# Performance work log

Measured on AMD Instinct MI355X. Metric: run time of the kernel, lower is better.

The kernel has to match this reference:

```python
import jax, jax.numpy as jnp
import numpy as np

N_NODES = 50000
N_EDGES = 1_600_000
N_HEADS = 8
IN_DIM = 512
OUT_DIM = 64
LRELU_ALPHA = 0.2


def setup_inputs() -> dict:
    key = jax.random.key(0)
    k1, k2, k3, k4, k5 = jax.random.split(key, 5)
    x = jax.random.normal(k1, (N_NODES, IN_DIM), dtype=jnp.float32)
    # glorot-ish scale for weights
    W = jax.random.normal(k2, (N_HEADS, IN_DIM, OUT_DIM), dtype=jnp.float32) * (1.0 / np.sqrt(IN_DIM))
    att_w = jax.random.normal(k3, (N_HEADS, 2 * OUT_DIM), dtype=jnp.float32) * (1.0 / np.sqrt(2 * OUT_DIM))
    src = jax.random.randint(k4, (N_EDGES,), 0, N_NODES, dtype=jnp.int64 if jax.config.read('jax_enable_x64') else jnp.int32).astype(jnp.int32)
    dst = jax.random.randint(k5, (N_EDGES,), 0, N_NODES, dtype=jnp.int32)
    return {"x": x, "W": W, "att_w": att_w, "src": src, "dst": dst}


def reference(x, W, att_w, src, dst):
    # GAT forward (eval mode: dropout=0, bias off, heads concatenated).
    # attention score: leaky_relu([f_src || f_dst] @ a) == leaky_relu(a1.f_src + a2.f_dst)
    outs = []
    for h in range(N_HEADS):
        feat = x @ W[h]                               # [N, F]
        a1 = att_w[h, :OUT_DIM]                       # [F]
        a2 = att_w[h, OUT_DIM:]                       # [F]
        alpha_s = feat @ a1                           # [N]
        alpha_d = feat @ a2                           # [N]
        logit = jax.nn.leaky_relu(alpha_s[src] + alpha_d[dst], LRELU_ALPHA)  # [E]
        # sparse row-wise softmax over segments keyed by src (row index)
        m = jax.ops.segment_max(logit, src, num_segments=N_NODES)
        e = jnp.exp(logit - m[src])
        denom = jax.ops.segment_sum(e, src, num_segments=N_NODES)
        att = e / denom[src]                          # [E]
        # sparse-dense aggregation: out[row] = sum_edges att * feat[col]
        agg = jax.ops.segment_sum(att[:, None] * feat[dst], src, num_segments=N_NODES)  # [N, F]
        outs.append(jax.nn.relu(agg))                 # act per head (average_heads=False)
    return jnp.concatenate(outs, axis=1)              # [N, H*F]
```

## Files before the change

kernel.cpp:

```cpp
#include <hip/hip_runtime.h>
#include <math.h>

#define N_NODES   50000
#define N_EDGES   1600000
#define N_HEADS   8
#define IN_DIM    512
#define OUT_DIM   64
#define FEAT_DIM  512
#define LRELU_A   0.2f
#define M_TILES   391
#define M_PAD     (M_TILES*128)

typedef __attribute__((ext_vector_type(8))) short bf16x8;
typedef __attribute__((ext_vector_type(4))) float f32x4;

__device__ inline unsigned short f2bf(float f) {
    unsigned int u = __float_as_uint(f);
    u = (u + 0x7FFFu + ((u >> 16) & 1u)) >> 16;
    return (unsigned short)u;
}
__device__ inline float bf2f(short s) {
    return __uint_as_float(((unsigned int)(unsigned short)s) << 16);
}

__global__ __launch_bounds__(256) void convert_x(const float* __restrict__ x,
                                                 unsigned short* __restrict__ xh) {
    int i = blockIdx.x * blockDim.x + threadIdx.x;
    if (i >= N_NODES * IN_DIM / 4) return;
    float4 v = ((const float4*)x)[i];
    ushort4 o;
    o.x = f2bf(v.x); o.y = f2bf(v.y); o.z = f2bf(v.z); o.w = f2bf(v.w);
    ((ushort4*)xh)[i] = o;
}

__global__ __launch_bounds__(256) void prep_b(const float* __restrict__ W,
                                              unsigned short* __restrict__ Bt) {
    int t = blockIdx.x * blockDim.x + threadIdx.x;
    if (t >= FEAT_DIM * IN_DIM) return;
    int n = t >> 9, k = t & 511;
    int h = n >> 6, o = n & 63;
    Bt[t] = f2bf(W[(size_t)h * IN_DIM * OUT_DIM + (size_t)k * OUT_DIM + o]);
}

__global__ __launch_bounds__(256) void gemm_mfma(const unsigned short* __restrict__ xh,
                                                 const unsigned short* __restrict__ Bt,
                                                 unsigned short* __restrict__ feat_h) {
    __shared__ __align__(16) unsigned short As[128 * 32];
    __shared__ __align__(16) unsigned short Bs[128 * 32];
    const int t    = threadIdx.x;
    const int wid  = t >> 6;
    const int lane = t & 63;
    const int m0   = blockIdx.x * 128;
    const int n0   = blockIdx.y * 128;
    const int wm   = (wid >> 1) * 64;
    const int wn   = (wid & 1) * 64;
    const int mr   = lane & 15;
    const int q    = lane >> 4;

    f32x4 acc[4][4];
    #pragma unroll
    for (int i = 0; i < 4; ++i)
        #pragma unroll
        for (int j = 0; j < 4; ++j) acc[i][j] = 0.0f;

    const char* xb = (const char*)xh;
    const char* bb = (const char*)Bt;
    const int o1 = t * 16;         const int row1 = o1 >> 6, kb1 = o1 & 63;
    const int o2 = t * 16 + 4096;  const int row2 = o2 >> 6, kb2 = o2 & 63;
    char* lA1 = ((char*)As) + wid * 1024;
    char* lA2 = ((char*)As) + 4096 + wid * 1024;
    char* lB1 = ((char*)Bs) + wid * 1024;
    char* lB2 = ((char*)Bs) + 4096 + wid * 1024;

    for (int k0 = 0; k0 < IN_DIM; k0 += 32) {
        const int kbyte = k0 * 2;
        __builtin_amdgcn_global_load_lds(
            (const __attribute__((address_space(1))) unsigned int*)(xb + (size_t)(m0 + row1) * (IN_DIM * 2) + kbyte + kb1),
            (__attribute__((address_space(3))) unsigned int*)lA1, 16, 0, 0);
        __builtin_amdgcn_global_load_lds(
            (const __attribute__((address_space(1))) unsigned int*)(xb + (size_t)(m0 + row2) * (IN_DIM * 2) + kbyte + kb2),
            (__attribute__((address_space(3))) unsigned int*)lA2, 16, 0, 0);
        __builtin_amdgcn_global_load_lds(
            (const __attribute__((address_space(1))) unsigned int*)(bb + (size_t)(n0 + row1) * (IN_DIM * 2) + kbyte + kb1),
            (__attribute__((address_space(3))) unsigned int*)lB1, 16, 0, 0);
        __builtin_amdgcn_global_load_lds(
            (const __attribute__((address_space(1))) unsigned int*)(bb + (size_t)(n0 + row2) * (IN_DIM * 2) + kbyte + kb2),
            (__attribute__((address_space(3))) unsigned int*)lB2, 16, 0, 0);
        __syncthreads();

        bf16x8 a[4], b[4];
        #pragma unroll
        for (int i = 0; i < 4; ++i)
            a[i] = *(const bf16x8*)&As[(wm + i * 16 + mr) * 32 + q * 8];
        #pragma unroll
        for (int j = 0; j < 4; ++j)
            b[j] = *(const bf16x8*)&Bs[(wn + j * 16 + mr) * 32 + q * 8];
        #pragma unroll
        for (int i = 0; i < 4; ++i)
            #pragma unroll
            for (int j = 0; j < 4; ++j)
                acc[i][j] = __builtin_amdgcn_mfma_f32_16x16x32_bf16(a[i], b[j], acc[i][j], 0, 0, 0);
        __syncthreads();
    }

    #pragma unroll
    for (int i = 0; i < 4; ++i) {
        #pragma unroll
        for (int j = 0; j < 4; ++j) {
            int col = n0 + wn + j * 16 + mr;
            #pragma unroll
            for (int r = 0; r < 4; ++r) {
                int row = m0 + wm + i * 16 + q * 4 + r;
                if (row < N_NODES)
                    feat_h[(size_t)row * FEAT_DIM + col] = f2bf(acc[i][j][r]);
            }
        }
    }
}

__global__ __launch_bounds__(256) void alpha_kernel(const unsigned short* __restrict__ feat_h,
                                                    const float* __restrict__ att_w,
                                                    float* __restrict__ alpha_s,
                                                    float* __restrict__ alpha_d) {
    int node = (blockIdx.x * blockDim.x + threadIdx.x) >> 6;
    int lane = threadIdx.x & 63;
    if (node >= N_NODES) return;
    int h   = lane >> 3;
    int sub = lane & 7;
    bf16x8 f = *(const bf16x8*)&feat_h[(size_t)node * FEAT_DIM + lane * 8];
    float s = 0.f, d = 0.f;
    #pragma unroll
    for (int i = 0; i < 8; ++i) {
        float fv = bf2f(f[i]);
        s += fv * att_w[h * 128 + sub * 8 + i];
        d += fv * att_w[h * 128 + 64 + sub * 8 + i];
    }
    #pragma unroll
    for (int off = 1; off < 8; off <<= 1) {
        s += __shfl_xor(s, off);
        d += __shfl_xor(d, off);
    }
    if (sub == 0) {
        alpha_s[node * N_HEADS + h] = s;
        alpha_d[node * N_HEADS + h] = d;
    }
}

__global__ __launch_bounds__(256) void count_kernel(const int* __restrict__ src,
                                                    int* __restrict__ cnt) {
    int e = blockIdx.x * blockDim.x + threadIdx.x;
    if (e < N_EDGES) atomicAdd(&cnt[src[e]], 1);
}

__global__ __launch_bounds__(1024) void scan_kernel(const int* __restrict__ cnt,
                                                    int* __restrict__ row_ptr,
                                                    int* __restrict__ cursor) {
    __shared__ int wsum[16];
    const int t    = threadIdx.x;
    const int lane = t & 63;
    const int wid  = t >> 6;
    int carry = 0;
    for (int base = 0; base < N_NODES; base += 1024) {
        int i = base + t;
        int v = (i < N_NODES) ? cnt[i] : 0;
        int incl = v;
        #pragma unroll
        for (int off = 1; off < 64; off <<= 1) {
            int u = __shfl_up(incl, off);
            if (lane >= off) incl += u;
        }
        if (lane == 63) wsum[wid] = incl;
        __syncthreads();
        if (t < 16) {
            int u = wsum[t];
            #pragma unroll
            for (int off = 1; off < 16; off <<= 1) {
                int w = __shfl_up(u, off);
                if (t >= off) u += w;
            }
            wsum[t] = u;
        }
        __syncthreads();
        int woff = (wid > 0) ? wsum[wid - 1] : 0;
        int excl = carry + woff + incl - v;
        if (i < N_NODES) { row_ptr[i] = excl; cursor[i] = excl; }
        carry += wsum[15];
        __syncthreads();
    }
    if (t == 0) row_ptr[N_NODES] = carry;
}

__global__ __launch_bounds__(256) void scatter_kernel(const int* __restrict__ src,
                                                      const int* __restrict__ dst,
                                                      int* __restrict__ cursor,
                                                      int* __restrict__ csr_dst) {
    int e = blockIdx.x * blockDim.x + threadIdx.x;
    if (e < N_EDGES) {
        int pos = atomicAdd(&cursor[src[e]], 1);
        csr_dst[pos] = dst[e];
    }
}

__global__ __launch_bounds__(256) void agg_kernel(const unsigned short* __restrict__ feat_h,
                                                  const float* __restrict__ alpha_s,
                                                  const float* __restrict__ alpha_d,
                                                  const int* __restrict__ row_ptr,
                                                  const int* __restrict__ csr_dst,
                                                  float* __restrict__ out) {
    const int node = (blockIdx.x * blockDim.x + threadIdx.x) >> 6;
    const int lane = threadIdx.x & 63;
    if (node >= N_NODES) return;
    const int h     = lane >> 3;
    const int start = row_ptr[node];
    const int deg   = row_ptr[node + 1] - start;
    const float as  = alpha_s[node * N_HEADS + h];
    const int* cd   = csr_dst + start;

    float sacc = 0.f;
    float acc[8] = {};

    int j = 0;
    for (; j + 4 <= deg; j += 4) {
        int d0 = cd[j + 0], d1 = cd[j + 1], d2 = cd[j + 2], d3 = cd[j + 3];
        float ad0 = alpha_d[d0 * N_HEADS + h];
        float ad1 = alpha_d[d1 * N_HEADS + h];
        float ad2 = alpha_d[d2 * N_HEADS + h];
        float ad3 = alpha_d[d3 * N_HEADS + h];
        bf16x8 f0 = *(const bf16x8*)&feat_h[(size_t)d0 * FEAT_DIM + lane * 8];
        bf16x8 f1 = *(const bf16x8*)&feat_h[(size_t)d1 * FEAT_DIM + lane * 8];
        bf16x8 f2 = *(const bf16x8*)&feat_h[(size_t)d2 * FEAT_DIM + lane * 8];
        bf16x8 f3 = *(const bf16x8*)&feat_h[(size_t)d3 * FEAT_DIM + lane * 8];
        float z0 = as + ad0; z0 = z0 > 0.f ? z0 : LRELU_A * z0; float e0 = __expf(z0);
        float z1 = as + ad1; z1 = z1 > 0.f ? z1 : LRELU_A * z1; float e1 = __expf(z1);
        float z2 = as + ad2; z2 = z2 > 0.f ? z2 : LRELU_A * z2; float e2 = __expf(z2);
        float z3 = as + ad3; z3 = z3 > 0.f ? z3 : LRELU_A * z3; float e3 = __expf(z3);
        sacc += (e0 + e1) + (e2 + e3);
        #pragma unroll
        for (int i = 0; i < 8; ++i) {
            acc[i] += e0 * bf2f(f0[i]);
            acc[i] += e1 * bf2f(f1[i]);
            acc[i] += e2 * bf2f(f2[i]);
            acc[i] += e3 * bf2f(f3[i]);
        }
    }
    for (; j < deg; ++j) {
        int d    = cd[j];
        float ad = alpha_d[d * N_HEADS + h];
        bf16x8 f = *(const bf16x8*)&feat_h[(size_t)d * FEAT_DIM + lane * 8];
        float z  = as + ad; z = z > 0.f ? z : LRELU_A * z;
        float e  = __expf(z);
        sacc += e;
        #pragma unroll
        for (int i = 0; i < 8; ++i)
            acc[i] += e * bf2f(f[i]);
    }

    const float inv = (deg > 0) ? 1.f / sacc : 0.f;
    f32x4 o0 = { fmaxf(acc[0] * inv, 0.f), fmaxf(acc[1] * inv, 0.f),
                 fmaxf(acc[2] * inv, 0.f), fmaxf(acc[3] * inv, 0.f) };
    f32x4 o1 = { fmaxf(acc[4] * inv, 0.f), fmaxf(acc[5] * inv, 0.f),
                 fmaxf(acc[6] * inv, 0.f), fmaxf(acc[7] * inv, 0.f) };
    f32x4* op = (f32x4*)(out + (size_t)node * FEAT_DIM + lane * 8);
    __builtin_nontemporal_store(o0, op);
    __builtin_nontemporal_store(o1, op + 1);
}

extern "C" void kernel_launch(void* const* d_in, const int* in_sizes, int n_in,
                              void* d_out, int out_size, void* d_ws, size_t ws_size,
                              hipStream_t stream) {
    const float* x     = (const float*)d_in[0];
    const float* W     = (const float*)d_in[1];
    const float* att_w = (const float*)d_in[2];
    const int*   src   = (const int*)d_in[3];
    const int*   dst   = (const int*)d_in[4];
    float* out = (float*)d_out;

    char* ws = (char*)d_ws;
    size_t off = 0;
    auto alloc = [&](size_t bytes) {
        void* p = ws + off;
        off += (bytes + 255) & ~(size_t)255;
        return p;
    };
    unsigned short* feat_h = (unsigned short*)alloc((size_t)N_NODES * FEAT_DIM * sizeof(short));
    unsigned short* xh     = (unsigned short*)alloc((size_t)M_PAD * IN_DIM * sizeof(short));
    unsigned short* Bt     = (unsigned short*)alloc((size_t)FEAT_DIM * IN_DIM * sizeof(short));
    float* alpha_s = (float*)alloc((size_t)N_NODES * N_HEADS * sizeof(float));
    float* alpha_d = (float*)alloc((size_t)N_NODES * N_HEADS * sizeof(float));
    int*   cnt     = (int*)alloc((size_t)N_NODES * sizeof(int));
    int*   row_ptr = (int*)alloc((size_t)(N_NODES + 1) * sizeof(int));
    int*   cursor  = (int*)alloc((size_t)N_NODES * sizeof(int));
    int*   csr_dst = (int*)alloc((size_t)N_EDGES * sizeof(int));

    (void)hipMemsetAsync(cnt, 0, (size_t)N_NODES * sizeof(int), stream);

    convert_x<<<(N_NODES * IN_DIM / 4 + 255) / 256, 256, 0, stream>>>(x, xh);
    prep_b<<<(FEAT_DIM * IN_DIM + 255) / 256, 256, 0, stream>>>(W, Bt);

    dim3 ggrid(M_TILES, FEAT_DIM / 128);
    gemm_mfma<<<ggrid, 256, 0, stream>>>(xh, Bt, feat_h);

    alpha_kernel<<<(N_NODES + 3) / 4, 256, 0, stream>>>(feat_h, att_w, alpha_s, alpha_d);

    count_kernel<<<(N_EDGES + 255) / 256, 256, 0, stream>>>(src, cnt);
    scan_kernel<<<1, 1024, 0, stream>>>(cnt, row_ptr, cursor);
    scatter_kernel<<<(N_EDGES + 255) / 256, 256, 0, stream>>>(src, dst, cursor, csr_dst);

    agg_kernel<<<(N_NODES * 64 + 255) / 256, 256, 0, stream>>>(feat_h, alpha_s, alpha_d, row_ptr, csr_dst, out);
}
```

Baseline: 730.1 us.

## Parallelize CSR scan, vectorize count/scatter, split agg rows across two waves

Replaces the single-block serial prefix scan with a three-kernel multi-block scan. The count and scatter kernels now process four edges per thread using int4 loads. The aggregation kernel gives each node two wavefronts, each covering half the edges with an 8-wide unrolled gather, and combines the halves through shared memory. The goal is to remove the serial scan bottleneck and expose more memory-level parallelism in the gather, at the cost of extra launches and a block-wide sync.

```diff
diff --git a/kernel.cpp b/kernel.cpp
--- a/kernel.cpp
+++ b/kernel.cpp
@@ -10,6 +10,7 @@
 #define LRELU_A   0.2f
 #define M_TILES   391
 #define M_PAD     (M_TILES*128)
+#define SCAN_BLK  49
 
 typedef __attribute__((ext_vector_type(8))) short bf16x8;
 typedef __attribute__((ext_vector_type(4))) float f32x4;
@@ -148,56 +149,96 @@
 
 __global__ __launch_bounds__(256) void count_kernel(const int* __restrict__ src,
                                                     int* __restrict__ cnt) {
-    int e = blockIdx.x * blockDim.x + threadIdx.x;
-    if (e < N_EDGES) atomicAdd(&cnt[src[e]], 1);
-}
-
-__global__ __launch_bounds__(1024) void scan_kernel(const int* __restrict__ cnt,
-                                                    int* __restrict__ row_ptr,
-                                                    int* __restrict__ cursor) {
+    int e = (blockIdx.x * blockDim.x + threadIdx.x) * 4;
+    if (e < N_EDGES) {
+        int4 s = *(const int4*)&src[e];
+        atomicAdd(&cnt[s.x], 1);
+        atomicAdd(&cnt[s.y], 1);
+        atomicAdd(&cnt[s.z], 1);
+        atomicAdd(&cnt[s.w], 1);
+    }
+}
+
+__global__ __launch_bounds__(1024) void scan_block_sums(const int* __restrict__ cnt,
+                                                        int* __restrict__ partials) {
     __shared__ int wsum[16];
     const int t    = threadIdx.x;
     const int lane = t & 63;
     const int wid  = t >> 6;
-    int carry = 0;
-    for (int base = 0; base < N_NODES; base += 1024) {
-        int i = base + t;
-        int v = (i < N_NODES) ? cnt[i] : 0;
-        int incl = v;
-        #pragma unroll
-        for (int off = 1; off < 64; off <<= 1) {
-            int u = __shfl_up(incl, off);
-            if (lane >= off) incl += u;
+    int i = blockIdx.x * 1024 + t;
+    int v = (i < N_NODES) ? cnt[i] : 0;
+    #pragma unroll
+    for (int off = 32; off > 0; off >>= 1) v += __shfl_xor(v, off);
+    if (lane == 0) wsum[wid] = v;
+    __syncthreads();
+    if (t < 16) {
+        int u = wsum[t];
+        #pragma unroll
+        for (int off = 1; off < 16; off <<= 1) u += __shfl_xor(u, off);
+        if (t == 0) partials[blockIdx.x] = u;
+    }
+}
+
+__global__ __launch_bounds__(64) void scan_partials(const int* __restrict__ partials,
+                                                    int* __restrict__ blkoff,
+                                                    int* __restrict__ row_ptr) {
+    int l = threadIdx.x;
+    int v = (l < SCAN_BLK) ? partials[l] : 0;
+    int incl = v;
+    #pragma unroll
+    for (int off = 1; off < 64; off <<= 1) {
+        int u = __shfl_up(incl, off);
+        if (l >= off) incl += u;
+    }
+    if (l < SCAN_BLK) blkoff[l] = incl - v;
+    if (l == SCAN_BLK - 1) row_ptr[N_NODES] = incl;
+}
+
+__global__ __launch_bounds__(1024) void scan_apply(const int* __restrict__ cnt,
+                                                   const int* __restrict__ blkoff,
+                                                   int* __restrict__ row_ptr,
+                                                   int* __restrict__ cursor) {
+    __shared__ int wsum[16];
+    const int t    = threadIdx.x;
+    const int lane = t & 63;
+    const int wid  = t >> 6;
+    int i = blockIdx.x * 1024 + t;
+    int v = (i < N_NODES) ? cnt[i] : 0;
+    int incl = v;
+    #pragma unroll
+    for (int off = 1; off < 64; off <<= 1) {
+        int u = __shfl_up(incl, off);
+        if (lane >= off) incl += u;
+    }
+    if (lane == 63) wsum[wid] = incl;
+    __syncthreads();
+    if (t < 16) {
+        int u = wsum[t];
+        #pragma unroll
+        for (int off = 1; off < 16; off <<= 1) {
+            int w = __shfl_up(u, off);
+            if (t >= off) u += w;
         }
-        if (lane == 63) wsum[wid] = incl;
-        __syncthreads();
-        if (t < 16) {
-            int u = wsum[t];
-            #pragma unroll
-            for (int off = 1; off < 16; off <<= 1) {
-                int w = __shfl_up(u, off);
-                if (t >= off) u += w;
-            }
-            wsum[t] = u;
-        }
-        __syncthreads();
-        int woff = (wid > 0) ? wsum[wid - 1] : 0;
-        int excl = carry + woff + incl - v;
-        if (i < N_NODES) { row_ptr[i] = excl; cursor[i] = excl; }
-        carry += wsum[15];
-        __syncthreads();
-    }
-    if (t == 0) row_ptr[N_NODES] = carry;
+        wsum[t] = u;
+    }
+    __syncthreads();
+    int woff = (wid > 0) ? wsum[wid - 1] : 0;
+    int excl = blkoff[blockIdx.x] + woff + incl - v;
+    if (i < N_NODES) { row_ptr[i] = excl; cursor[i] = excl; }
 }
 
 __global__ __launch_bounds__(256) void scatter_kernel(const int* __restrict__ src,
                                                       const int* __restrict__ dst,
                                                       int* __restrict__ cursor,
                                                       int* __restrict__ csr_dst) {
-    int e = blockIdx.x * blockDim.x + threadIdx.x;
+    int e = (blockIdx.x * blockDim.x + threadIdx.x) * 4;
     if (e < N_EDGES) {
-        int pos = atomicAdd(&cursor[src[e]], 1);
-        csr_dst[pos] = dst[e];
+        int4 s = *(const int4*)&src[e];
+        int4 d = *(const int4*)&dst[e];
+        int p0 = atomicAdd(&cursor[s.x], 1); csr_dst[p0] = d.x;
+        int p1 = atomicAdd(&cursor[s.y], 1); csr_dst[p1] = d.y;
+        int p2 = atomicAdd(&cursor[s.z], 1); csr_dst[p2] = d.z;
+        int p3 = atomicAdd(&cursor[s.w], 1); csr_dst[p3] = d.w;
     }
 }
 
@@ -207,62 +248,84 @@
                                                   const int* __restrict__ row_ptr,
                                                   const int* __restrict__ csr_dst,
                                                   float* __restrict__ out) {
-    const int node = (blockIdx.x * blockDim.x + threadIdx.x) >> 6;
+    __shared__ float red[2][64][9];
+    const int wv   = __builtin_amdgcn_readfirstlane(threadIdx.x >> 6);
     const int lane = threadIdx.x & 63;
-    if (node >= N_NODES) return;
-    const int h     = lane >> 3;
+    const int node = blockIdx.x * 2 + (wv >> 1);
+    const int half = wv & 1;
+    const int h    = lane >> 3;
+
     const int start = row_ptr[node];
-    const int deg   = row_ptr[node + 1] - start;
+    const int end   = row_ptr[node + 1];
+    const int deg   = end - start;
+    const int lo    = start + ((deg * half) >> 1);
+    const int hi    = start + ((deg * (half + 1)) >> 1);
+    const int cnt2  = hi - lo;
     const float as  = alpha_s[node * N_HEADS + h];
-    const int* cd   = csr_dst + start;
+    const int* cd   = csr_dst + lo;
 
     float sacc = 0.f;
     float acc[8] = {};
 
     int j = 0;
-    for (; j + 4 <= deg; j += 4) {
-        int d0 = cd[j + 0], d1 = cd[j + 1], d2 = cd[j + 2], d3 = cd[j + 3];
-        float ad0 = alpha_d[d0 * N_HEADS + h];
-        float ad1 = alpha_d[d1 * N_HEADS + h];
-        float ad2 = alpha_d[d2 * N_HEADS + h];
-        float ad3 = alpha_d[d3 * N_HEADS + h];
-        bf16x8 f0 = *(const bf16x8*)&feat_h[(size_t)d0 * FEAT_DIM + lane * 8];
-        bf16x8 f1 = *(const bf16x8*)&feat_h[(size_t)d1 * FEAT_DIM + lane * 8];
-        bf16x8 f2 = *(const bf16x8*)&feat_h[(size_t)d2 * FEAT_DIM + lane * 8];
-        bf16x8 f3 = *(const bf16x8*)&feat_h[(size_t)d3 * FEAT_DIM + lane * 8];
-        float z0 = as + ad0; z0 = z0 > 0.f ? z0 : LRELU_A * z0; float e0 = __expf(z0);
-        float z1 = as + ad1; z1 = z1 > 0.f ? z1 : LRELU_A * z1; float e1 = __expf(z1);
-        float z2 = as + ad2; z2 = z2 > 0.f ? z2 : LRELU_A * z2; float e2 = __expf(z2);
-        float z3 = as + ad3; z3 = z3 > 0.f ? z3 : LRELU_A * z3; float e3 = __expf(z3);
-        sacc += (e0 + e1) + (e2 + e3);
+    for (; j + 8 <= cnt2; j += 8) {
+        int d[8];
+        #pragma unroll
+        for (int k = 0; k < 8; ++k) d[k] = cd[j + k];
+        float ad[8];
+        #pragma unroll
+        for (int k = 0; k < 8; ++k) ad[k] = alpha_d[(size_t)d[k] * N_HEADS + h];
+        bf16x8 f[8];
+        #pragma unroll
+        for (int k = 0; k < 8; ++k)
+            f[k] = *(const bf16x8*)&feat_h[(size_t)d[k] * FEAT_DIM + lane * 8];
+        float e[8];
+        #pragma unroll
+        for (int k = 0; k < 8; ++k) {
+            float z = as + ad[k];
+            z = z > 0.f ? z : LRELU_A * z;
+            e[k] = __expf(z);
+        }
+        sacc += ((e[0] + e[1]) + (e[2] + e[3])) + ((e[4] + e[5]) + (e[6] + e[7]));
         #pragma unroll
         for (int i = 0; i < 8; ++i) {
-            acc[i] += e0 * bf2f(f0[i]);
-            acc[i] += e1 * bf2f(f1[i]);
-            acc[i] += e2 * bf2f(f2[i]);
-            acc[i] += e3 * bf2f(f3[i]);
+            float a = acc[i];
+            #pragma unroll
+            for (int k = 0; k < 8; ++k) a += e[k] * bf2f(f[k][i]);
+            acc[i] = a;
         }
     }
-    for (; j < deg; ++j) {
-        int d    = cd[j];
-        float ad = alpha_d[d * N_HEADS + h];
-        bf16x8 f = *(const bf16x8*)&feat_h[(size_t)d * FEAT_DIM + lane * 8];
-        float z  = as + ad; z = z > 0.f ? z : LRELU_A * z;
-        float e  = __expf(z);
-        sacc += e;
-        #pragma unroll
-        for (int i = 0; i < 8; ++i)
-            acc[i] += e * bf2f(f[i]);
-    }
-
-    const float inv = (deg > 0) ? 1.f / sacc : 0.f;
-    f32x4 o0 = { fmaxf(acc[0] * inv, 0.f), fmaxf(acc[1] * inv, 0.f),
-                 fmaxf(acc[2] * inv, 0.f), fmaxf(acc[3] * inv, 0.f) };
-    f32x4 o1 = { fmaxf(acc[4] * inv, 0.f), fmaxf(acc[5] * inv, 0.f),
-                 fmaxf(acc[6] * inv, 0.f), fmaxf(acc[7] * inv, 0.f) };
-    f32x4* op = (f32x4*)(out + (size_t)node * FEAT_DIM + lane * 8);
-    __builtin_nontemporal_store(o0, op);
-    __builtin_nontemporal_store(o1, op + 1);
+    for (; j < cnt2; ++j) {
+        int dd = cd[j];
+        float ad0 = alpha_d[(size_t)dd * N_HEADS + h];
+        bf16x8 f0 = *(const bf16x8*)&feat_h[(size_t)dd * FEAT_DIM + lane * 8];
+        float z = as + ad0; z = z > 0.f ? z : LRELU_A * z;
+        float e0 = __expf(z);
+        sacc += e0;
+        #pragma unroll
+        for (int i = 0; i < 8; ++i) acc[i] += e0 * bf2f(f0[i]);
+    }
+
+    const int pr = wv >> 1;
+    if (half == 1) {
+        #pragma unroll
+        for (int i = 0; i < 8; ++i) red[pr][lane][i] = acc[i];
+        red[pr][lane][8] = sacc;
+    }
+    __syncthreads();
+    if (half == 0) {
+        #pragma unroll
+        for (int i = 0; i < 8; ++i) acc[i] += red[pr][lane][i];
+        sacc += red[pr][lane][8];
+        const float inv = (deg > 0) ? 1.f / sacc : 0.f;
+        f32x4 o0 = { fmaxf(acc[0] * inv, 0.f), fmaxf(acc[1] * inv, 0.f),
+                     fmaxf(acc[2] * inv, 0.f), fmaxf(acc[3] * inv, 0.f) };
+        f32x4 o1 = { fmaxf(acc[4] * inv, 0.f), fmaxf(acc[5] * inv, 0.f),
+                     fmaxf(acc[6] * inv, 0.f), fmaxf(acc[7] * inv, 0.f) };
+        f32x4* op = (f32x4*)(out + (size_t)node * FEAT_DIM + lane * 8);
+        __builtin_nontemporal_store(o0, op);
+        __builtin_nontemporal_store(o1, op + 1);
+    }
 }
 
 extern "C" void kernel_launch(void* const* d_in, const int* in_sizes, int n_in,
@@ -291,6 +354,8 @@
     int*   row_ptr = (int*)alloc((size_t)(N_NODES + 1) * sizeof(int));
     int*   cursor  = (int*)alloc((size_t)N_NODES * sizeof(int));
     int*   csr_dst = (int*)alloc((size_t)N_EDGES * sizeof(int));
+    int*   partials = (int*)alloc((size_t)SCAN_BLK * sizeof(int));
+    int*   blkoff   = (int*)alloc((size_t)SCAN_BLK * sizeof(int));
 
     (void)hipMemsetAsync(cnt, 0, (size_t)N_NODES * sizeof(int), stream);
 
@@ -302,9 +367,11 @@
 
     alpha_kernel<<<(N_NODES + 3) / 4, 256, 0, stream>>>(feat_h, att_w, alpha_s, alpha_d);
 
-    count_kernel<<<(N_EDGES + 255) / 256, 256, 0, stream>>>(src, cnt);
-    scan_kernel<<<1, 1024, 0, stream>>>(cnt, row_ptr, cursor);
-    scatter_kernel<<<(N_EDGES + 255) / 256, 256, 0, stream>>>(src, dst, cursor, csr_dst);
-
-    agg_kernel<<<(N_NODES * 64 + 255) / 256, 256, 0, stream>>>(feat_h, alpha_s, alpha_d, row_ptr, csr_dst, out);
-}
+    count_kernel<<<(N_EDGES / 4 + 255) / 256, 256, 0, stream>>>(src, cnt);
+    scan_block_sums<<<SCAN_BLK, 1024, 0, stream>>>(cnt, partials);
+    scan_partials<<<1, 64, 0, stream>>>(partials, blkoff, row_ptr);
+    scan_apply<<<SCAN_BLK, 1024, 0, stream>>>(cnt, blkoff, row_ptr, cursor);
+    scatter_kernel<<<(N_EDGES / 4 + 255) / 256, 256, 0, stream>>>(src, dst, cursor, csr_dst);
+
+    agg_kernel<<<N_NODES / 2, 256, 0, stream>>>(feat_h, alpha_s, alpha_d, row_ptr, csr_dst, out);
+}
```

New measurement: 685.2 us. 6.1% less time.
